# Optimization experiments

Measured on AMD Instinct MI355X. Metric: run time of the kernel, lower is better.

Reference implementation:

```python
import jax, jax.numpy as jnp
import numpy as np

BETA = 1.0  # init kwarg beta


def setup_inputs() -> dict:
    key = jax.random.key(0)
    k1, k2 = jax.random.split(key)
    B, K = 8192, 64
    policy_logps = jax.random.normal(k1, (B, K), dtype=jnp.float32)
    reward_scores = jax.random.uniform(k2, (B, K), dtype=jnp.float32)
    return {"policy_logps": policy_logps, "reward_scores": reward_scores}


def reference(policy_logps, reward_scores):
    B, K = policy_logps.shape
    s = policy_logps  # rf_free=True -> scores = policy_logps
    r = reward_scores

    # ranks: 1-based rank of each item when rewards sorted descending
    order = jnp.argsort(-r, axis=-1)              # [B, K]
    ranks = jnp.argsort(order, axis=-1) + 1        # [B, K]
    inv_discount = 1.0 / jnp.log1p(ranks.astype(s.dtype))  # [B, K]
    gain = 2.0 * r - 1.0                            # [B, K]

    # pairwise matrices [B, K, K]; loop in original covers i > j (strict lower triangle)
    delta = jnp.abs(gain[:, :, None] - gain[:, None, :]) * \
            jnp.abs(inv_discount[:, :, None] - inv_discount[:, None, :])
    diff = s[:, :, None] - s[:, None, :]
    term = delta * jax.nn.log_sigmoid(-BETA * diff)

    mask = jnp.tril(jnp.ones((K, K), dtype=bool), k=-1)  # i > j
    loss_sum = jnp.sum(jnp.where(mask[None], term, 0.0))
    count = B * (K * (K - 1) // 2)
    return -loss_sum / count
```

## Files before the change

### kernel.cpp

```cpp
#include <hip/hip_runtime.h>

typedef float v2f __attribute__((ext_vector_type(2)));

#define KDIM 64
#define WAVES_PER_BLOCK 4
#define ROWS_PER_WAVE 2
#define ROWS_PER_BLOCK (WAVES_PER_BLOCK * ROWS_PER_WAVE)

#define LOG2E 1.44269504088896f

__device__ __forceinline__ v2f pair_term(v2f g2, v2f d2, v2f s2,
                                         v2f gj, v2f dj, v2f sj, float qc) {
    v2f pd = (g2 - gj) * (d2 - dj);
    v2f del; del.x = fabsf(pd.x); del.y = fabsf(pd.y);
    v2f u = qc * (s2 - sj);
    v2f e; e.x = __builtin_amdgcn_exp2f(u.x); e.y = __builtin_amdgcn_exp2f(u.y);
    v2f le = 1.0f + e;
    v2f l; l.x = __builtin_amdgcn_logf(le.x); l.y = __builtin_amdgcn_logf(le.y);
    return del * l;
}

template <int CTRL>
__device__ __forceinline__ float dpp_qperm(float x) {
    return __uint_as_float((unsigned int)__builtin_amdgcn_update_dpp(
        0, (int)__float_as_uint(x), CTRL, 0xF, 0xF, true));
}
#define QROT1 0x93
#define QROT2 0x4E

__global__ __launch_bounds__(256) void rankdpo_main(
    const float* __restrict__ s_in, const float* __restrict__ r_in,
    float* __restrict__ partials, int B)
{
    const int wave = threadIdx.x >> 6;
    const int lane = threadIdx.x & 63;
    const int qi = lane >> 2;
    const int bi = lane & 3;

    const int row0 = blockIdx.x * ROWS_PER_BLOCK + wave * ROWS_PER_WAVE;
    const int row1 = row0 + 1;
    const int a0 = (row0 < B ? row0 : 0) * KDIM + lane;
    const int a1 = (row1 < B ? row1 : 0) * KDIM + lane;

    const float s0 = s_in[a0], r0 = r_in[a0];
    const float s1 = s_in[a1], r1 = r_in[a1];

    __shared__ __align__(16) v2f sh[WAVES_PER_BLOCK][4][128];
    v2f* rbuf = sh[wave][0];
    v2f* sbuf = sh[wave][1];
    v2f* gbuf = sh[wave][2];
    v2f* dbuf = sh[wave][3];

    rbuf[lane] = v2f{r0, r1};  rbuf[lane + 64] = v2f{r0, r1};
    sbuf[lane] = v2f{s0, s1};  sbuf[lane + 64] = v2f{s0, s1};

    int c0 = 0, c1 = 0;
    #pragma unroll
    for (int t = 0; t < 16; ++t) {
        float4 qa = *(const float4*)&rbuf[4 * t];
        float4 qb = *(const float4*)&rbuf[4 * t + 2];
        c0 += (qa.x > r0) + (qa.z > r0) + (qb.x > r0) + (qb.z > r0);
        c1 += (qa.y > r1) + (qa.w > r1) + (qb.y > r1) + (qb.w > r1);
    }
    const float invd0 = __builtin_amdgcn_rcpf(__builtin_amdgcn_logf((float)(c0 + 2)));
    const float invd1 = __builtin_amdgcn_rcpf(__builtin_amdgcn_logf((float)(c1 + 2)));
    const float g0 = 2.0f * r0 - 1.0f;
    const float g1 = 2.0f * r1 - 1.0f;

    gbuf[lane] = v2f{g0, g1};        gbuf[lane + 64] = v2f{g0, g1};
    dbuf[lane] = v2f{invd0, invd1};  dbuf[lane + 64] = v2f{invd0, invd1};

    const v2f s2 = {s0, s1}, g2 = {g0, g1}, d2 = {invd0, invd1};
    v2f p = {0.0f, 0.0f};

    const float keep8 = (qi >= 8) ? 1.0f : 0.0f;
    #pragma unroll
    for (int t = 1; t <= 8; ++t) {
        const int Q = (qi + 16 - t) << 2;
        float4 sa = *(const float4*)&sbuf[Q], sb = *(const float4*)&sbuf[Q + 2];
        float4 ga = *(const float4*)&gbuf[Q], gb = *(const float4*)&gbuf[Q + 2];
        float4 da = *(const float4*)&dbuf[Q], db = *(const float4*)&dbuf[Q + 2];
        const float qc = (qi >= t) ? LOG2E : -LOG2E;

        v2f term = pair_term(g2, d2, s2, v2f{ga.x, ga.y}, v2f{da.x, da.y}, v2f{sa.x, sa.y}, qc);
        term = term + pair_term(g2, d2, s2, v2f{ga.z, ga.w}, v2f{da.z, da.w}, v2f{sa.z, sa.w}, qc);
        term = term + pair_term(g2, d2, s2, v2f{gb.x, gb.y}, v2f{db.x, db.y}, v2f{sb.x, sb.y}, qc);
        term = term + pair_term(g2, d2, s2, v2f{gb.z, gb.w}, v2f{db.z, db.w}, v2f{sb.z, sb.w}, qc);
        if (t == 8) term = term * keep8;
        p = p + term;
    }

    {
        const float qcA = (bi >= 1) ? LOG2E : -LOG2E;
        const float keepB = (bi >= 2) ? 1.0f : 0.0f;

        v2f sjA = {dpp_qperm<QROT1>(s0), dpp_qperm<QROT1>(s1)};
        v2f gjA = {dpp_qperm<QROT1>(g0), dpp_qperm<QROT1>(g1)};
        v2f djA = {dpp_qperm<QROT1>(invd0), dpp_qperm<QROT1>(invd1)};
        v2f sjB = {dpp_qperm<QROT2>(s0), dpp_qperm<QROT2>(s1)};
        v2f gjB = {dpp_qperm<QROT2>(g0), dpp_qperm<QROT2>(g1)};
        v2f djB = {dpp_qperm<QROT2>(invd0), dpp_qperm<QROT2>(invd1)};

        p = p + pair_term(g2, d2, s2, gjA, djA, sjA, qcA);
        p = p + pair_term(g2, d2, s2, gjB, djB, sjB, LOG2E) * keepB;
    }

    if (row0 >= B) p.x = 0.0f;
    if (row1 >= B) p.y = 0.0f;

    float pacc = p.x + p.y;
    #pragma unroll
    for (int off = 32; off > 0; off >>= 1)
        pacc += __shfl_down(pacc, off);

    __shared__ float wsum[WAVES_PER_BLOCK];
    if (lane == 0) wsum[wave] = pacc;
    __syncthreads();
    if (threadIdx.x == 0)
        partials[blockIdx.x] = wsum[0] + wsum[1] + wsum[2] + wsum[3];
}

__global__ __launch_bounds__(256) void rankdpo_reduce(
    const float* __restrict__ partials, int n, float* __restrict__ out,
    double inv_count)
{
    double sum = 0.0;
    for (int i = threadIdx.x; i < n; i += 256)
        sum += (double)partials[i];
    __shared__ double sh[256];
    sh[threadIdx.x] = sum;
    __syncthreads();
    for (int st = 128; st > 0; st >>= 1) {
        if (threadIdx.x < st) sh[threadIdx.x] += sh[threadIdx.x + st];
        __syncthreads();
    }
    if (threadIdx.x == 0)
        out[0] = (float)(sh[0] * inv_count);
}

extern "C" void kernel_launch(void* const* d_in, const int* in_sizes, int n_in,
                              void* d_out, int out_size, void* d_ws, size_t ws_size,
                              hipStream_t stream) {
    const float* s = (const float*)d_in[0];
    const float* r = (const float*)d_in[1];
    float* out = (float*)d_out;

    const int BK = in_sizes[0];
    const int B  = BK / KDIM;
    const int nblocks = (B + ROWS_PER_BLOCK - 1) / ROWS_PER_BLOCK;

    float* partials = (float*)d_ws;

    const long long count = (long long)B * (KDIM * (KDIM - 1) / 2);
    const double inv_count = 1.0 / (double)count;

    rankdpo_main<<<nblocks, 256, 0, stream>>>(s, r, partials, B);
    rankdpo_reduce<<<1, 256, 0, stream>>>(partials, nblocks, out, inv_count);
}
```

Measured before the change: 66.11 us.

## Split each row pair's pairwise work across two waves

Each row pair is now handled by two waves, and each wave covers half of the 8 shifted chunks of pairwise terms. This doubles the grid to 2048 blocks, giving more parallelism and shorter per-wave dependency chains. The cost is that every wave redoes the loads, rank counting and shared-memory setup for its rows, which doubles global reads and rank work. The rank buffer also drops its unused duplicated half, shrinking LDS use.

```diff
diff --git a/kernel.cpp b/kernel.cpp
--- a/kernel.cpp
+++ b/kernel.cpp
@@ -4,8 +4,6 @@
 
 #define KDIM 64
 #define WAVES_PER_BLOCK 4
-#define ROWS_PER_WAVE 2
-#define ROWS_PER_BLOCK (WAVES_PER_BLOCK * ROWS_PER_WAVE)
 
 #define LOG2E 1.44269504088896f
 
@@ -28,6 +26,21 @@
 #define QROT1 0x93
 #define QROT2 0x4E
 
+__device__ __forceinline__ v2f chunk(const v2f* sbuf, const v2f* gbuf,
+                                     const v2f* dbuf, int qi, int t,
+                                     v2f s2, v2f g2, v2f d2) {
+    const int Q = (qi + 16 - t) << 2;
+    float4 sa = *(const float4*)&sbuf[Q], sb = *(const float4*)&sbuf[Q + 2];
+    float4 ga = *(const float4*)&gbuf[Q], gb = *(const float4*)&gbuf[Q + 2];
+    float4 da = *(const float4*)&dbuf[Q], db = *(const float4*)&dbuf[Q + 2];
+    const float qc = (qi >= t) ? LOG2E : -LOG2E;
+    v2f term = pair_term(g2, d2, s2, v2f{ga.x, ga.y}, v2f{da.x, da.y}, v2f{sa.x, sa.y}, qc);
+    term = term + pair_term(g2, d2, s2, v2f{ga.z, ga.w}, v2f{da.z, da.w}, v2f{sa.z, sa.w}, qc);
+    term = term + pair_term(g2, d2, s2, v2f{gb.x, gb.y}, v2f{db.x, db.y}, v2f{sb.x, sb.y}, qc);
+    term = term + pair_term(g2, d2, s2, v2f{gb.z, gb.w}, v2f{db.z, db.w}, v2f{sb.z, sb.w}, qc);
+    return term;
+}
+
 __global__ __launch_bounds__(256) void rankdpo_main(
     const float* __restrict__ s_in, const float* __restrict__ r_in,
     float* __restrict__ partials, int B)
@@ -37,7 +50,10 @@
     const int qi = lane >> 2;
     const int bi = lane & 3;
 
-    const int row0 = blockIdx.x * ROWS_PER_BLOCK + wave * ROWS_PER_WAVE;
+    const int wave_id = blockIdx.x * WAVES_PER_BLOCK + wave;
+    const int rp = wave_id >> 1;
+    const int h  = wave_id & 1;
+    const int row0 = 2 * rp;
     const int row1 = row0 + 1;
     const int a0 = (row0 < B ? row0 : 0) * KDIM + lane;
     const int a1 = (row1 < B ? row1 : 0) * KDIM + lane;
@@ -45,13 +61,16 @@
     const float s0 = s_in[a0], r0 = r_in[a0];
     const float s1 = s_in[a1], r1 = r_in[a1];
 
-    __shared__ __align__(16) v2f sh[WAVES_PER_BLOCK][4][128];
-    v2f* rbuf = sh[wave][0];
-    v2f* sbuf = sh[wave][1];
-    v2f* gbuf = sh[wave][2];
-    v2f* dbuf = sh[wave][3];
+    __shared__ __align__(16) v2f shs[WAVES_PER_BLOCK][128];
+    __shared__ __align__(16) v2f shg[WAVES_PER_BLOCK][128];
+    __shared__ __align__(16) v2f shd[WAVES_PER_BLOCK][128];
+    __shared__ __align__(16) v2f shr[WAVES_PER_BLOCK][64];
+    v2f* sbuf = shs[wave];
+    v2f* gbuf = shg[wave];
+    v2f* dbuf = shd[wave];
+    v2f* rbuf = shr[wave];
 
-    rbuf[lane] = v2f{r0, r1};  rbuf[lane + 64] = v2f{r0, r1};
+    rbuf[lane] = v2f{r0, r1};
     sbuf[lane] = v2f{s0, s1};  sbuf[lane + 64] = v2f{s0, s1};
 
     int c0 = 0, c1 = 0;
@@ -73,34 +92,26 @@
     const v2f s2 = {s0, s1}, g2 = {g0, g1}, d2 = {invd0, invd1};
     v2f p = {0.0f, 0.0f};
 
-    const float keep8 = (qi >= 8) ? 1.0f : 0.0f;
-    #pragma unroll
-    for (int t = 1; t <= 8; ++t) {
-        const int Q = (qi + 16 - t) << 2;
-        float4 sa = *(const float4*)&sbuf[Q], sb = *(const float4*)&sbuf[Q + 2];
-        float4 ga = *(const float4*)&gbuf[Q], gb = *(const float4*)&gbuf[Q + 2];
-        float4 da = *(const float4*)&dbuf[Q], db = *(const float4*)&dbuf[Q + 2];
-        const float qc = (qi >= t) ? LOG2E : -LOG2E;
+    if (h == 0) {
+        p = p + chunk(sbuf, gbuf, dbuf, qi, 1, s2, g2, d2);
+        p = p + chunk(sbuf, gbuf, dbuf, qi, 2, s2, g2, d2);
+        p = p + chunk(sbuf, gbuf, dbuf, qi, 3, s2, g2, d2);
+        p = p + chunk(sbuf, gbuf, dbuf, qi, 4, s2, g2, d2);
+    } else {
+        p = p + chunk(sbuf, gbuf, dbuf, qi, 5, s2, g2, d2);
+        p = p + chunk(sbuf, gbuf, dbuf, qi, 6, s2, g2, d2);
+        p = p + chunk(sbuf, gbuf, dbuf, qi, 7, s2, g2, d2);
+        const float keep8 = (qi >= 8) ? 1.0f : 0.0f;
+        p = p + chunk(sbuf, gbuf, dbuf, qi, 8, s2, g2, d2) * keep8;
 
-        v2f term = pair_term(g2, d2, s2, v2f{ga.x, ga.y}, v2f{da.x, da.y}, v2f{sa.x, sa.y}, qc);
-        term = term + pair_term(g2, d2, s2, v2f{ga.z, ga.w}, v2f{da.z, da.w}, v2f{sa.z, sa.w}, qc);
-        term = term + pair_term(g2, d2, s2, v2f{gb.x, gb.y}, v2f{db.x, db.y}, v2f{sb.x, sb.y}, qc);
-        term = term + pair_term(g2, d2, s2, v2f{gb.z, gb.w}, v2f{db.z, db.w}, v2f{sb.z, sb.w}, qc);
-        if (t == 8) term = term * keep8;
-        p = p + term;
-    }
-
-    {
         const float qcA = (bi >= 1) ? LOG2E : -LOG2E;
         const float keepB = (bi >= 2) ? 1.0f : 0.0f;
-
         v2f sjA = {dpp_qperm<QROT1>(s0), dpp_qperm<QROT1>(s1)};
         v2f gjA = {dpp_qperm<QROT1>(g0), dpp_qperm<QROT1>(g1)};
         v2f djA = {dpp_qperm<QROT1>(invd0), dpp_qperm<QROT1>(invd1)};
         v2f sjB = {dpp_qperm<QROT2>(s0), dpp_qperm<QROT2>(s1)};
         v2f gjB = {dpp_qperm<QROT2>(g0), dpp_qperm<QROT2>(g1)};
         v2f djB = {dpp_qperm<QROT2>(invd0), dpp_qperm<QROT2>(invd1)};
-
         p = p + pair_term(g2, d2, s2, gjA, djA, sjA, qcA);
         p = p + pair_term(g2, d2, s2, gjB, djB, sjB, LOG2E) * keepB;
     }
@@ -147,7 +158,9 @@
 
     const int BK = in_sizes[0];
     const int B  = BK / KDIM;
-    const int nblocks = (B + ROWS_PER_BLOCK - 1) / ROWS_PER_BLOCK;
+    const int npairs = (B + 1) / 2;
+    const int nwaves = 2 * npairs;
+    const int nblocks = (nwaves + WAVES_PER_BLOCK - 1) / WAVES_PER_BLOCK;
 
     float* partials = (float*)d_ws;
 
```

Measured after the change: 68.15 us. +3.1%, slower.

## Process four rows per wave and fold gain scaling into final constant

Applied to the files above, without the earlier changes.

Each wave now handles four rows as two packed pairs instead of two, interleaving two independent pair-term streams to raise instruction-level parallelism and halve the block count. The gain buffer is dropped: since |(2r_i-1)-(2r_j-1)| = 2|r_i-r_j|, raw rewards are used and the factor of two moves into inv_count. This cuts LDS traffic and per-pair arithmetic, at the cost of more registers and LDS per wave and fewer waves in flight.

```diff
diff --git a/kernel.cpp b/kernel.cpp
--- a/kernel.cpp
+++ b/kernel.cpp
@@ -4,14 +4,14 @@
 
 #define KDIM 64
 #define WAVES_PER_BLOCK 4
-#define ROWS_PER_WAVE 2
+#define ROWS_PER_WAVE 4
 #define ROWS_PER_BLOCK (WAVES_PER_BLOCK * ROWS_PER_WAVE)
 
 #define LOG2E 1.44269504088896f
 
-__device__ __forceinline__ v2f pair_term(v2f g2, v2f d2, v2f s2,
-                                         v2f gj, v2f dj, v2f sj, float qc) {
-    v2f pd = (g2 - gj) * (d2 - dj);
+__device__ __forceinline__ v2f pair_term(v2f r2, v2f d2, v2f s2,
+                                         v2f rj, v2f dj, v2f sj, float qc) {
+    v2f pd = (r2 - rj) * (d2 - dj);
     v2f del; del.x = fabsf(pd.x); del.y = fabsf(pd.y);
     v2f u = qc * (s2 - sj);
     v2f e; e.x = __builtin_amdgcn_exp2f(u.x); e.y = __builtin_amdgcn_exp2f(u.y);
@@ -28,6 +28,21 @@
 #define QROT1 0x93
 #define QROT2 0x4E
 
+__device__ __forceinline__ v2f chunk(const v2f* sbuf, const v2f* rbuf,
+                                     const v2f* dbuf, int qi, int t,
+                                     v2f s2, v2f r2, v2f d2) {
+    const int Q = (qi + 16 - t) << 2;
+    float4 sa = *(const float4*)&sbuf[Q], sb = *(const float4*)&sbuf[Q + 2];
+    float4 ra = *(const float4*)&rbuf[Q], rb = *(const float4*)&rbuf[Q + 2];
+    float4 da = *(const float4*)&dbuf[Q], db = *(const float4*)&dbuf[Q + 2];
+    const float qc = (qi >= t) ? LOG2E : -LOG2E;
+    v2f term = pair_term(r2, d2, s2, v2f{ra.x, ra.y}, v2f{da.x, da.y}, v2f{sa.x, sa.y}, qc);
+    term = term + pair_term(r2, d2, s2, v2f{ra.z, ra.w}, v2f{da.z, da.w}, v2f{sa.z, sa.w}, qc);
+    term = term + pair_term(r2, d2, s2, v2f{rb.x, rb.y}, v2f{db.x, db.y}, v2f{sb.x, sb.y}, qc);
+    term = term + pair_term(r2, d2, s2, v2f{rb.z, rb.w}, v2f{db.z, db.w}, v2f{sb.z, sb.w}, qc);
+    return term;
+}
+
 __global__ __launch_bounds__(256) void rankdpo_main(
     const float* __restrict__ s_in, const float* __restrict__ r_in,
     float* __restrict__ partials, int B)
@@ -37,78 +52,89 @@
     const int qi = lane >> 2;
     const int bi = lane & 3;
 
-    const int row0 = blockIdx.x * ROWS_PER_BLOCK + wave * ROWS_PER_WAVE;
-    const int row1 = row0 + 1;
+    const int base = (blockIdx.x * WAVES_PER_BLOCK + wave) * ROWS_PER_WAVE;
+    const int row0 = base, row1 = base + 1, row2 = base + 2, row3 = base + 3;
     const int a0 = (row0 < B ? row0 : 0) * KDIM + lane;
     const int a1 = (row1 < B ? row1 : 0) * KDIM + lane;
+    const int a2 = (row2 < B ? row2 : 0) * KDIM + lane;
+    const int a3 = (row3 < B ? row3 : 0) * KDIM + lane;
 
     const float s0 = s_in[a0], r0 = r_in[a0];
     const float s1 = s_in[a1], r1 = r_in[a1];
+    const float s2s = s_in[a2], r2s = r_in[a2];
+    const float s3 = s_in[a3], r3 = r_in[a3];
 
-    __shared__ __align__(16) v2f sh[WAVES_PER_BLOCK][4][128];
-    v2f* rbuf = sh[wave][0];
-    v2f* sbuf = sh[wave][1];
-    v2f* gbuf = sh[wave][2];
-    v2f* dbuf = sh[wave][3];
+    __shared__ __align__(16) v2f sh[WAVES_PER_BLOCK][6][128];
+    v2f* sA = sh[wave][0]; v2f* rA = sh[wave][1]; v2f* dA = sh[wave][2];
+    v2f* sB = sh[wave][3]; v2f* rB = sh[wave][4]; v2f* dB = sh[wave][5];
 
-    rbuf[lane] = v2f{r0, r1};  rbuf[lane + 64] = v2f{r0, r1};
-    sbuf[lane] = v2f{s0, s1};  sbuf[lane + 64] = v2f{s0, s1};
+    sA[lane] = v2f{s0, s1};   sA[lane + 64] = v2f{s0, s1};
+    rA[lane] = v2f{r0, r1};   rA[lane + 64] = v2f{r0, r1};
+    sB[lane] = v2f{s2s, s3};  sB[lane + 64] = v2f{s2s, s3};
+    rB[lane] = v2f{r2s, r3};  rB[lane + 64] = v2f{r2s, r3};
 
-    int c0 = 0, c1 = 0;
+    int c0 = 0, c1 = 0, c2 = 0, c3 = 0;
     #pragma unroll
     for (int t = 0; t < 16; ++t) {
-        float4 qa = *(const float4*)&rbuf[4 * t];
-        float4 qb = *(const float4*)&rbuf[4 * t + 2];
+        float4 qa = *(const float4*)&rA[4 * t];
+        float4 qb = *(const float4*)&rA[4 * t + 2];
+        float4 qc4 = *(const float4*)&rB[4 * t];
+        float4 qd = *(const float4*)&rB[4 * t + 2];
         c0 += (qa.x > r0) + (qa.z > r0) + (qb.x > r0) + (qb.z > r0);
         c1 += (qa.y > r1) + (qa.w > r1) + (qb.y > r1) + (qb.w > r1);
+        c2 += (qc4.x > r2s) + (qc4.z > r2s) + (qd.x > r2s) + (qd.z > r2s);
+        c3 += (qc4.y > r3) + (qc4.w > r3) + (qd.y > r3) + (qd.w > r3);
     }
     const float invd0 = __builtin_amdgcn_rcpf(__builtin_amdgcn_logf((float)(c0 + 2)));
     const float invd1 = __builtin_amdgcn_rcpf(__builtin_amdgcn_logf((float)(c1 + 2)));
-    const float g0 = 2.0f * r0 - 1.0f;
-    const float g1 = 2.0f * r1 - 1.0f;
+    const float invd2 = __builtin_amdgcn_rcpf(__builtin_amdgcn_logf((float)(c2 + 2)));
+    const float invd3 = __builtin_amdgcn_rcpf(__builtin_amdgcn_logf((float)(c3 + 2)));
 
-    gbuf[lane] = v2f{g0, g1};        gbuf[lane + 64] = v2f{g0, g1};
-    dbuf[lane] = v2f{invd0, invd1};  dbuf[lane + 64] = v2f{invd0, invd1};
+    dA[lane] = v2f{invd0, invd1};  dA[lane + 64] = v2f{invd0, invd1};
+    dB[lane] = v2f{invd2, invd3};  dB[lane + 64] = v2f{invd2, invd3};
 
-    const v2f s2 = {s0, s1}, g2 = {g0, g1}, d2 = {invd0, invd1};
-    v2f p = {0.0f, 0.0f};
+    const v2f sa2 = {s0, s1},  ra2 = {r0, r1},  da2 = {invd0, invd1};
+    const v2f sb2 = {s2s, s3}, rb2 = {r2s, r3}, db2 = {invd2, invd3};
+    v2f pA = {0.0f, 0.0f}, pB = {0.0f, 0.0f};
 
     const float keep8 = (qi >= 8) ? 1.0f : 0.0f;
     #pragma unroll
-    for (int t = 1; t <= 8; ++t) {
-        const int Q = (qi + 16 - t) << 2;
-        float4 sa = *(const float4*)&sbuf[Q], sb = *(const float4*)&sbuf[Q + 2];
-        float4 ga = *(const float4*)&gbuf[Q], gb = *(const float4*)&gbuf[Q + 2];
-        float4 da = *(const float4*)&dbuf[Q], db = *(const float4*)&dbuf[Q + 2];
-        const float qc = (qi >= t) ? LOG2E : -LOG2E;
-
-        v2f term = pair_term(g2, d2, s2, v2f{ga.x, ga.y}, v2f{da.x, da.y}, v2f{sa.x, sa.y}, qc);
-        term = term + pair_term(g2, d2, s2, v2f{ga.z, ga.w}, v2f{da.z, da.w}, v2f{sa.z, sa.w}, qc);
-        term = term + pair_term(g2, d2, s2, v2f{gb.x, gb.y}, v2f{db.x, db.y}, v2f{sb.x, sb.y}, qc);
-        term = term + pair_term(g2, d2, s2, v2f{gb.z, gb.w}, v2f{db.z, db.w}, v2f{sb.z, sb.w}, qc);
-        if (t == 8) term = term * keep8;
-        p = p + term;
+    for (int t = 1; t <= 7; ++t) {
+        pA = pA + chunk(sA, rA, dA, qi, t, sa2, ra2, da2);
+        pB = pB + chunk(sB, rB, dB, qi, t, sb2, rb2, db2);
     }
+    pA = pA + chunk(sA, rA, dA, qi, 8, sa2, ra2, da2) * keep8;
+    pB = pB + chunk(sB, rB, dB, qi, 8, sb2, rb2, db2) * keep8;
 
     {
         const float qcA = (bi >= 1) ? LOG2E : -LOG2E;
         const float keepB = (bi >= 2) ? 1.0f : 0.0f;
 
-        v2f sjA = {dpp_qperm<QROT1>(s0), dpp_qperm<QROT1>(s1)};
-        v2f gjA = {dpp_qperm<QROT1>(g0), dpp_qperm<QROT1>(g1)};
-        v2f djA = {dpp_qperm<QROT1>(invd0), dpp_qperm<QROT1>(invd1)};
-        v2f sjB = {dpp_qperm<QROT2>(s0), dpp_qperm<QROT2>(s1)};
-        v2f gjB = {dpp_qperm<QROT2>(g0), dpp_qperm<QROT2>(g1)};
-        v2f djB = {dpp_qperm<QROT2>(invd0), dpp_qperm<QROT2>(invd1)};
+        v2f sj1A = {dpp_qperm<QROT1>(s0), dpp_qperm<QROT1>(s1)};
+        v2f rj1A = {dpp_qperm<QROT1>(r0), dpp_qperm<QROT1>(r1)};
+        v2f dj1A = {dpp_qperm<QROT1>(invd0), dpp_qperm<QROT1>(invd1)};
+        v2f sj1B = {dpp_qperm<QROT1>(s2s), dpp_qperm<QROT1>(s3)};
+        v2f rj1B = {dpp_qperm<QROT1>(r2s), dpp_qperm<QROT1>(r3)};
+        v2f dj1B = {dpp_qperm<QROT1>(invd2), dpp_qperm<QROT1>(invd3)};
+        pA = pA + pair_term(ra2, da2, sa2, rj1A, dj1A, sj1A, qcA);
+        pB = pB + pair_term(rb2, db2, sb2, rj1B, dj1B, sj1B, qcA);
 
-        p = p + pair_term(g2, d2, s2, gjA, djA, sjA, qcA);
-        p = p + pair_term(g2, d2, s2, gjB, djB, sjB, LOG2E) * keepB;
+        v2f sj2A = {dpp_qperm<QROT2>(s0), dpp_qperm<QROT2>(s1)};
+        v2f rj2A = {dpp_qperm<QROT2>(r0), dpp_qperm<QROT2>(r1)};
+        v2f dj2A = {dpp_qperm<QROT2>(invd0), dpp_qperm<QROT2>(invd1)};
+        v2f sj2B = {dpp_qperm<QROT2>(s2s), dpp_qperm<QROT2>(s3)};
+        v2f rj2B = {dpp_qperm<QROT2>(r2s), dpp_qperm<QROT2>(r3)};
+        v2f dj2B = {dpp_qperm<QROT2>(invd2), dpp_qperm<QROT2>(invd3)};
+        pA = pA + pair_term(ra2, da2, sa2, rj2A, dj2A, sj2A, LOG2E) * keepB;
+        pB = pB + pair_term(rb2, db2, sb2, rj2B, dj2B, sj2B, LOG2E) * keepB;
     }
 
-    if (row0 >= B) p.x = 0.0f;
-    if (row1 >= B) p.y = 0.0f;
+    if (row0 >= B) pA.x = 0.0f;
+    if (row1 >= B) pA.y = 0.0f;
+    if (row2 >= B) pB.x = 0.0f;
+    if (row3 >= B) pB.y = 0.0f;
 
-    float pacc = p.x + p.y;
+    float pacc = (pA.x + pA.y) + (pB.x + pB.y);
     #pragma unroll
     for (int off = 32; off > 0; off >>= 1)
         pacc += __shfl_down(pacc, off);
@@ -152,7 +178,7 @@
     float* partials = (float*)d_ws;
 
     const long long count = (long long)B * (KDIM * (KDIM - 1) / 2);
-    const double inv_count = 1.0 / (double)count;
+    const double inv_count = 2.0 / (double)count;
 
     rankdpo_main<<<nblocks, 256, 0, stream>>>(s, r, partials, B);
     rankdpo_reduce<<<1, 256, 0, stream>>>(partials, nblocks, out, inv_count);
```

New measurement: 66.10 us. No clear change (-0.0%).
